# Kernel tuning notes

Hardware: AMD Instinct MI355X
Metric: run time of the kernel (lower is better)

The kernel has to match this reference:

```python
import jax, jax.numpy as jnp
import numpy as np

B, S, D, H, FF = 2, 2048, 1024, 16, 4096
DH = D // H
EPS = 1e-5


def _linear_params(key, din, dout):
    kw, kb = jax.random.split(key)
    lim = 1.0 / np.sqrt(din)
    W = jax.random.uniform(kw, (din, dout), jnp.float32, -lim, lim)
    b = jax.random.uniform(kb, (dout,), jnp.float32, -lim, lim)
    return W, b


def setup_inputs() -> dict:
    key = jax.random.key(0)
    ks = jax.random.split(key, 8)
    x = jax.random.normal(ks[0], (B, S, D), jnp.float32)
    mask = jnp.ones((B, 1, 1, S), jnp.int32)
    wq, bq = _linear_params(ks[1], D, D)
    wk, bk = _linear_params(ks[2], D, D)
    wv, bv = _linear_params(ks[3], D, D)
    w1, b1 = _linear_params(ks[4], D, D)       # linear1 (attn output proj)
    fw1, fb1 = _linear_params(ks[5], D, FF)    # ffn.w_1
    fw2, fb2 = _linear_params(ks[6], FF, D)    # ffn.w_2
    g1 = jnp.ones((D,), jnp.float32); be1 = jnp.zeros((D,), jnp.float32)
    g2 = jnp.ones((D,), jnp.float32); be2 = jnp.zeros((D,), jnp.float32)
    return dict(x=x, mask=mask, wq=wq, bq=bq, wk=wk, bk=bk, wv=wv, bv=bv,
                w1=w1, b1=b1, g1=g1, be1=be1,
                fw1=fw1, fb1=fb1, fw2=fw2, fb2=fb2, g2=g2, be2=be2)


def _layernorm(x, g, b):
    mu = jnp.mean(x, axis=-1, keepdims=True)
    var = jnp.mean(jnp.square(x - mu), axis=-1, keepdims=True)
    return (x - mu) * jax.lax.rsqrt(var + EPS) * g + b


def _encoder(x, mask, wq, bq, wk, bk, wv, bv, w1, b1, g1, be1,
             fw1, fb1, fw2, fb2, g2, be2):
    res = x
    # QKV projections, reshape to [B, H, S, DH]
    q = (x @ wq + bq).reshape(B, S, H, DH).transpose(0, 2, 1, 3)
    k = (x @ wk + bk).reshape(B, S, H, DH).transpose(0, 2, 1, 3)
    v = (x @ wv + bv).reshape(B, S, H, DH).transpose(0, 2, 1, 3)
    scores = jnp.einsum('bhqd,bhkd->bhqk', q, k) / np.sqrt(DH).astype(np.float32)
    scores = jnp.where(mask == 0, jnp.float32(-1e9), scores)
    probs = jax.nn.softmax(scores, axis=-1)  # dropout = identity in eval
    attn = jnp.einsum('bhqk,bhkd->bhqd', probs, v)
    attn = attn.transpose(0, 2, 1, 3).reshape(B, S, D)
    x = _layernorm(attn @ w1 + b1 + res, g1, be1)
    res = x
    ff = jax.nn.relu(x @ fw1 + fb1) @ fw2 + fb2
    return _layernorm(ff + res, g2, be2)


def reference(x, mask, wq, bq, wk, bk, wv, bv, w1, b1, g1, be1,
              fw1, fb1, fw2, fb2, g2, be2):
    return _encoder(x, mask, wq, bq, wk, bk, wv, bv, w1, b1, g1, be1,
                    fw1, fb1, fw2, fb2, g2, be2)
```

## Files before the change

### kernel.cpp

```cpp
#include <hip/hip_runtime.h>
#include <hip/hip_bf16.h>
#include <cstdint>

typedef unsigned short u16;
typedef __attribute__((ext_vector_type(8))) short bf16x8;
typedef __attribute__((ext_vector_type(4))) float f32x4;

#define DEVFN static __device__ __forceinline__

static constexpr int S   = 2048;
static constexpr int D   = 1024;
static constexpr int DHd = 64;
static constexpr int FFd = 4096;
static constexpr int M   = 4096;
static constexpr int LDQ = 3072;

static constexpr float SC2 = 0.18033688f;

DEVFN u16 f2b(float v) {
    union { __hip_bfloat16 h; u16 u; } x;
    x.h = __float2bfloat16(v);
    return x.u;
}

typedef const uint32_t __attribute__((address_space(1)))* gptr_t;
typedef uint32_t __attribute__((address_space(3)))* lptr_t;
DEVFN void load16(const void* g, void* l) {
    __builtin_amdgcn_global_load_lds((gptr_t)g, (lptr_t)l, 16, 0, 0);
}

template<int MODE>
__global__ __launch_bounds__(512, 2)
void gemm256(const u16* __restrict__ A, const u16* __restrict__ BT,
             const float* __restrict__ bias, u16* __restrict__ outp, int N)
{
    constexpr int K = 1024;
    __shared__ __align__(16) u16 Lds[65536];
    const int tid  = threadIdx.x;
    const int lane = tid & 63;
    const int w    = tid >> 6;
    const int wm = w >> 2, wn = w & 3;
    const int g = lane >> 4, c = lane & 15;
    const int c7 = c & 7;
    const int bn0 = blockIdx.x * 256;
    const int bm0 = blockIdx.y * 256;

    const int sr = tid >> 3;
    const int gl = (tid & 7) ^ (sr & 7);
    const u16* Asrc = A  + (size_t)(bm0 + sr) * K + gl * 8;
    const u16* Bsrc = BT + (size_t)(bn0 + sr) * K + gl * 8;
    char* dA = (char*)Lds + (size_t)tid * 16;
    char* dB = dA + 32768;

#define STG_A(BUF, H, KT)                                                       \
    { _Pragma("unroll") for (int Lh = 0; Lh < 2; ++Lh)                          \
        load16(Asrc + (size_t)((H)*128 + Lh*64) * K + (KT)*64,                  \
               dA + (BUF)*65536 + (H)*16384 + Lh*8192); }
#define STG_B(BUF, H, KT)                                                       \
    { _Pragma("unroll") for (int Lh = 0; Lh < 2; ++Lh)                          \
        load16(Bsrc + (size_t)((H)*128 + Lh*64) * K + (KT)*64,                  \
               dB + (BUF)*65536 + (H)*16384 + Lh*8192); }
#define VMCNT(N_) asm volatile("s_waitcnt vmcnt(" #N_ ")" ::: "memory")
#define BAR() { __builtin_amdgcn_s_barrier(); __builtin_amdgcn_sched_barrier(0); }

    const char* lbase = (const char*)Lds;
    auto rdA = [&](int buf, int i, int kk) -> bf16x8 {
        const int half = i >> 2;
        const int lr = (2*(i & 3) + wm) * 16 + c;
        return *(const bf16x8*)(lbase + buf*65536 + half*16384 + lr*128
                                + (((kk<<2) + g) ^ c7) * 16);
    };
    auto rdB = [&](int buf, int j, int kk) -> bf16x8 {
        const int half = j >> 1;
        const int lr = (j & 1)*64 + wn*16 + c;
        return *(const bf16x8*)(lbase + buf*65536 + 32768 + half*16384 + lr*128
                                + (((kk<<2) + g) ^ c7) * 16);
    };

    const f32x4 fz = {0.f, 0.f, 0.f, 0.f};
    f32x4 acc[8][4];
#pragma unroll
    for (int i = 0; i < 8; ++i)
#pragma unroll
        for (int j = 0; j < 4; ++j) acc[i][j] = fz;

    bf16x8 af[4][2], bf[4][2];

    auto body = [&](int cur, int nxt, int kt, bool stage) {
        if (stage) STG_A(nxt, 0, kt + 1);
#pragma unroll
        for (int i = 0; i < 4; ++i)
#pragma unroll
            for (int kk = 0; kk < 2; ++kk) af[i][kk] = rdA(cur, i, kk);
#pragma unroll
        for (int j = 0; j < 2; ++j)
#pragma unroll
            for (int kk = 0; kk < 2; ++kk) bf[j][kk] = rdB(cur, j, kk);
        __builtin_amdgcn_s_setprio(1);
#pragma unroll
        for (int i = 0; i < 4; ++i)
#pragma unroll
            for (int j = 0; j < 2; ++j)
#pragma unroll
                for (int kk = 0; kk < 2; ++kk)
                    acc[i][j] = __builtin_amdgcn_mfma_f32_16x16x32_bf16(
                        af[i][kk], bf[j][kk], acc[i][j], 0, 0, 0);
        __builtin_amdgcn_s_setprio(0);
        if (stage) { VMCNT(4); } else { VMCNT(2); }
        BAR();
        if (stage) STG_B(nxt, 0, kt + 1);
#pragma unroll
        for (int j = 2; j < 4; ++j)
#pragma unroll
            for (int kk = 0; kk < 2; ++kk) bf[j][kk] = rdB(cur, j, kk);
        __builtin_amdgcn_s_setprio(1);
#pragma unroll
        for (int i = 0; i < 4; ++i)
#pragma unroll
            for (int j = 2; j < 4; ++j)
#pragma unroll
                for (int kk = 0; kk < 2; ++kk)
                    acc[i][j] = __builtin_amdgcn_mfma_f32_16x16x32_bf16(
                        af[i][kk], bf[j][kk], acc[i][j], 0, 0, 0);
        __builtin_amdgcn_s_setprio(0);
        if (stage) { VMCNT(4); } else { VMCNT(0); }
        BAR();
        if (stage) STG_B(nxt, 1, kt + 1);
#pragma unroll
        for (int i = 4; i < 8; ++i)
#pragma unroll
            for (int kk = 0; kk < 2; ++kk) af[i - 4][kk] = rdA(cur, i, kk);
        __builtin_amdgcn_s_setprio(1);
#pragma unroll
        for (int i = 4; i < 8; ++i)
#pragma unroll
            for (int j = 0; j < 2; ++j)
#pragma unroll
                for (int kk = 0; kk < 2; ++kk)
                    acc[i][j] = __builtin_amdgcn_mfma_f32_16x16x32_bf16(
                        af[i - 4][kk], bf[j][kk], acc[i][j], 0, 0, 0);
        __builtin_amdgcn_s_setprio(0);
        if (stage) STG_A(nxt, 1, kt + 1);
        __builtin_amdgcn_s_setprio(1);
#pragma unroll
        for (int i = 4; i < 8; ++i)
#pragma unroll
            for (int j = 2; j < 4; ++j)
#pragma unroll
                for (int kk = 0; kk < 2; ++kk)
                    acc[i][j] = __builtin_amdgcn_mfma_f32_16x16x32_bf16(
                        af[i - 4][kk], bf[j][kk], acc[i][j], 0, 0, 0);
        __builtin_amdgcn_s_setprio(0);
        if (stage) { VMCNT(4); BAR(); }
    };

    STG_A(0, 0, 0); STG_B(0, 0, 0); STG_B(0, 1, 0); STG_A(0, 1, 0);
    VMCNT(4);
    BAR();

#pragma unroll 1
    for (int kt = 0; kt < 14; kt += 2) {
        body(0, 1, kt, true);
        body(1, 0, kt + 1, true);
    }
    body(0, 1, 14, true);
    body(1, 0, 15, false);
#undef STG_A
#undef STG_B
#undef VMCNT
#undef BAR

#pragma unroll
    for (int i = 0; i < 8; ++i) {
        const int fm = (i >> 2) * 8 + (i & 3) * 2 + wm;
        const int row = bm0 + fm * 16 + 4 * g;
#pragma unroll
        for (int j = 0; j < 4; ++j) {
            const int fn = (j >> 1) * 8 + (j & 1) * 4 + wn;
            const int col = bn0 + fn * 16 + c;
            const float bv = bias[col];
            const float sc = (MODE == 3 && col < D) ? SC2 : 1.f;
#pragma unroll
            for (int r = 0; r < 4; ++r) {
                float v = acc[i][j][r] + bv;
                if (MODE == 2) v = v > 0.f ? v : 0.f;
                v *= sc;
                outp[(size_t)(row + r) * N + col] = f2b(v);
            }
        }
    }
}

template<int KTOT>
__global__ __launch_bounds__(256, 3)
void gemm_splitk(const u16* __restrict__ A, const u16* __restrict__ BT,
                 float* __restrict__ part)
{
    __shared__ __align__(16) u16 As[128 * 64];
    __shared__ __align__(16) u16 Bs[128 * 64];
    const int tid  = threadIdx.x;
    const int lane = tid & 63;
    const int w    = tid >> 6;
    const int wm = w >> 1, wn = w & 1;
    const int g = lane >> 4, c = lane & 15;
    const int bn0 = blockIdx.x * 128;
    const int bm0 = blockIdx.y * 128;
    const int z   = blockIdx.z;
    const int srow = tid >> 3;
    const int scol = (tid & 7) * 8;

    const f32x4 fz = {0.f, 0.f, 0.f, 0.f};
    f32x4 acc[4][4];
#pragma unroll
    for (int i = 0; i < 4; ++i)
#pragma unroll
        for (int j = 0; j < 4; ++j) acc[i][j] = fz;

    const u16* Ab = A  + (size_t)(bm0 + srow) * KTOT + z * (KTOT/2) + scol;
    const u16* Bb = BT + (size_t)(bn0 + srow) * KTOT + z * (KTOT/2) + scol;
    char* AsB = (char*)As + (size_t)tid * 16;
    char* BsB = (char*)Bs + (size_t)tid * 16;

    for (int kt = 0; kt < KTOT/128; ++kt) {
        const int k0 = kt << 6;
        __syncthreads();
#pragma unroll
        for (int cc = 0; cc < 4; ++cc) {
            load16(Ab + (size_t)(cc * 32) * KTOT + k0, AsB + cc * 4096);
            load16(Bb + (size_t)(cc * 32) * KTOT + k0, BsB + cc * 4096);
        }
        __syncthreads();
#pragma unroll
        for (int kk = 0; kk < 2; ++kk) {
            bf16x8 af[4], bfv[4];
#pragma unroll
            for (int i = 0; i < 4; ++i)
                af[i] = *(const bf16x8*)&As[(wm*64 + i*16 + c) * 64 + kk*32 + g*8];
#pragma unroll
            for (int j = 0; j < 4; ++j)
                bfv[j] = *(const bf16x8*)&Bs[(wn*64 + j*16 + c) * 64 + kk*32 + g*8];
#pragma unroll
            for (int i = 0; i < 4; ++i)
#pragma unroll
                for (int j = 0; j < 4; ++j)
                    acc[i][j] = __builtin_amdgcn_mfma_f32_16x16x32_bf16(
                        af[i], bfv[j], acc[i][j], 0, 0, 0);
        }
    }

    float* outz = part + (size_t)z * M * D;
#pragma unroll
    for (int i = 0; i < 4; ++i) {
        const int row = bm0 + wm*64 + i*16 + g*4;
#pragma unroll
        for (int j = 0; j < 4; ++j) {
            const int col = bn0 + wn*64 + j*16 + c;
#pragma unroll
            for (int r = 0; r < 4; ++r)
                outz[(size_t)(row + r) * D + col] = acc[i][j][r];
        }
    }
}

__global__ __launch_bounds__(256)
void ln_part_fused(const float* __restrict__ part, const float* __restrict__ bias,
                   const float* __restrict__ resid, const float* __restrict__ gam,
                   const float* __restrict__ bet, u16* __restrict__ out_b,
                   float* __restrict__ out_f)
{
    const int row = blockIdx.x;
    const int tid = threadIdx.x;
    __shared__ float red1[4], red2[4];
    const float4 p0 = ((const float4*)(part + (size_t)row * D))[tid];
    const float4 p1 = ((const float4*)(part + (size_t)(M + row) * D))[tid];
    const float4 bv = ((const float4*)bias)[tid];
    const float4 rv = ((const float4*)(resid + (size_t)row * D))[tid];
    const float y0 = p0.x + p1.x + bv.x + rv.x;
    const float y1 = p0.y + p1.y + bv.y + rv.y;
    const float y2 = p0.z + p1.z + bv.z + rv.z;
    const float y3 = p0.w + p1.w + bv.w + rv.w;
    float s1 = y0 + y1 + y2 + y3;
#pragma unroll
    for (int off = 1; off < 64; off <<= 1) s1 += __shfl_xor(s1, off);
    if ((tid & 63) == 0) red1[tid >> 6] = s1;
    __syncthreads();
    const float mu = (red1[0] + red1[1] + red1[2] + red1[3]) * (1.f / 1024.f);
    const float d0 = y0 - mu, d1 = y1 - mu, d2 = y2 - mu, d3 = y3 - mu;
    float s2 = d0*d0 + d1*d1 + d2*d2 + d3*d3;
#pragma unroll
    for (int off = 1; off < 64; off <<= 1) s2 += __shfl_xor(s2, off);
    if ((tid & 63) == 0) red2[tid >> 6] = s2;
    __syncthreads();
    const float var = (red2[0] + red2[1] + red2[2] + red2[3]) * (1.f / 1024.f);
    const float rs = rsqrtf(var + 1e-5f);
    const int c0 = tid * 4;
    const float o0 = d0 * rs * gam[c0+0] + bet[c0+0];
    const float o1 = d1 * rs * gam[c0+1] + bet[c0+1];
    const float o2 = d2 * rs * gam[c0+2] + bet[c0+2];
    const float o3 = d3 * rs * gam[c0+3] + bet[c0+3];
    if (out_b) {
        union { u16 u[4]; uint2 v; } pk;
        pk.u[0] = f2b(o0); pk.u[1] = f2b(o1); pk.u[2] = f2b(o2); pk.u[3] = f2b(o3);
        ((uint2*)(out_b + (size_t)row * D))[tid] = pk.v;
    }
    if (out_f) {
        float4 yv; yv.x = o0; yv.y = o1; yv.z = o2; yv.w = o3;
        ((float4*)(out_f + (size_t)row * D))[tid] = yv;
    }
}

__global__ __launch_bounds__(256, 3)
void attn_fwd9(const u16* __restrict__ QKV, const u16* __restrict__ VT,
               u16* __restrict__ Ob)
{
    __shared__ __align__(16) u16 Ks[3][64 * 64];
    __shared__ __align__(16) u16 Vs[3][64 * 64];
    __shared__ __align__(16) u16 Ps[4][32 * 72];
    const int tid  = threadIdx.x;
    const int lane = tid & 63;
    const int w    = tid >> 6;
    const int g = lane >> 4, c = lane & 15;
    const int bh = blockIdx.y;
    const int b = bh >> 4, h = bh & 15;
    const int q0 = blockIdx.x * 128 + w * 32;

    const u16* Qb = QKV;
    const u16* Kb = QKV + 1024;

    bf16x8 aq[2][2];
#pragma unroll
    for (int rt = 0; rt < 2; ++rt)
#pragma unroll
        for (int kk = 0; kk < 2; ++kk)
            aq[rt][kk] = *(const bf16x8*)&Qb[(size_t)(b*S + q0 + rt*16 + c) * LDQ
                                             + h*DHd + kk*32 + g*8];

    const f32x4 fz = {0.f, 0.f, 0.f, 0.f};
    const short one_b = (short)0x3F80;
    const bf16x8 onesv = {one_b, one_b, one_b, one_b, one_b, one_b, one_b, one_b};
    f32x4 o[2][4];
    f32x4 ol[2];
#pragma unroll
    for (int rt = 0; rt < 2; ++rt) {
        ol[rt] = fz;
#pragma unroll
        for (int j = 0; j < 4; ++j) o[rt][j] = fz;
    }

    const int sr = tid >> 3;
    const int glog = (tid & 7) ^ (sr & 7);
    const u16* Ksrc = Kb + (size_t)(b*S + sr) * LDQ + h*DHd + glog*8;
    const u16* Vsrc = VT + (size_t)(bh*DHd + sr) * S + glog*8;
    char* Kd0 = (char*)&Ks[0][0] + (size_t)tid * 16;
    char* Vd0 = (char*)&Vs[0][0] + (size_t)tid * 16;

#define STAGE(BUFI, kt_)                                                        \
    {                                                                           \
        const int kr0_ = (kt_) * 64;                                            \
        _Pragma("unroll")                                                       \
        for (int cc = 0; cc < 2; ++cc) {                                        \
            load16(Ksrc + (size_t)(kr0_ + cc*32) * LDQ, Kd0 + (BUFI)*8192 + cc*4096); \
            load16(Vsrc + (size_t)(cc*32) * S + kr0_,   Vd0 + (BUFI)*8192 + cc*4096); \
        }                                                                       \
    }
#define WAITBAR(N)                                                              \
    {                                                                           \
        asm volatile("s_waitcnt vmcnt(" #N ")" ::: "memory");                   \
        __builtin_amdgcn_s_barrier();                                           \
        __builtin_amdgcn_sched_barrier(0);                                      \
    }

    u16* pw = &Ps[w][0];
    const int c7 = c & 7;

    auto tile_body = [&](const u16* K0, const u16* V0) {
        bf16x8 bk[4][2];
#pragma unroll
        for (int j = 0; j < 4; ++j)
#pragma unroll
            for (int kk = 0; kk < 2; ++kk)
                bk[j][kk] = *(const bf16x8*)&K0[(j*16 + c) * 64 + (((kk<<2)+g) ^ c7) * 8];

#pragma unroll
        for (int rt = 0; rt < 2; ++rt) {
            f32x4 sv[4];
            __builtin_amdgcn_s_setprio(1);
#pragma unroll
            for (int j = 0; j < 4; ++j) {
                sv[j] = fz;
#pragma unroll
                for (int kk = 0; kk < 2; ++kk)
                    sv[j] = __builtin_amdgcn_mfma_f32_16x16x32_bf16(
                        bk[j][kk], aq[rt][kk], sv[j], 0, 0, 0);
            }
            __builtin_amdgcn_s_setprio(0);

#pragma unroll
            for (int j = 0; j < 4; ++j) {
                const float p0 = exp2f(sv[j][0]);
                const float p1 = exp2f(sv[j][1]);
                const float p2 = exp2f(sv[j][2]);
                const float p3 = exp2f(sv[j][3]);
                union { u16 u[4]; uint2 v; } pk;
                pk.u[0] = f2b(p0); pk.u[1] = f2b(p1);
                pk.u[2] = f2b(p2); pk.u[3] = f2b(p3);
                *(uint2*)&pw[(rt*16 + c) * 72 + j*16 + g*4] = pk.v;
            }
        }

        __builtin_amdgcn_s_setprio(1);
#pragma unroll
        for (int st = 0; st < 2; ++st) {
            bf16x8 bv[4];
#pragma unroll
            for (int j = 0; j < 4; ++j)
                bv[j] = *(const bf16x8*)&V0[(j*16 + c) * 64 + (((st<<2)+g) ^ c7) * 8];
#pragma unroll
            for (int rt = 0; rt < 2; ++rt) {
                const bf16x8 ap = *(const bf16x8*)&pw[(rt*16 + c) * 72 + st*32 + g*8];
#pragma unroll
                for (int j = 0; j < 4; ++j)
                    o[rt][j] = __builtin_amdgcn_mfma_f32_16x16x32_bf16(
                        ap, bv[j], o[rt][j], 0, 0, 0);
                ol[rt] = __builtin_amdgcn_mfma_f32_16x16x32_bf16(
                    ap, onesv, ol[rt], 0, 0, 0);
            }
        }
        __builtin_amdgcn_s_setprio(0);
    };

    STAGE(0, 0);
    STAGE(1, 1);
    WAITBAR(4);

    int kt = 0;
#pragma unroll 1
    for (int it = 0; it < 10; ++it, kt += 3) {
        STAGE(2, kt + 2); tile_body(&Ks[0][0], &Vs[0][0]); WAITBAR(4);
        STAGE(0, kt + 3); tile_body(&Ks[1][0], &Vs[1][0]); WAITBAR(4);
        STAGE(1, kt + 4); tile_body(&Ks[2][0], &Vs[2][0]); WAITBAR(4);
    }
    tile_body(&Ks[0][0], &Vs[0][0]); WAITBAR(0);
    tile_body(&Ks[1][0], &Vs[1][0]);
#undef STAGE
#undef WAITBAR

#pragma unroll
    for (int rt = 0; rt < 2; ++rt) {
#pragma unroll
        for (int r = 0; r < 4; ++r) {
            const float rl = __builtin_amdgcn_rcpf(ol[rt][r]);
            const size_t row = (size_t)(b*S + q0 + rt*16 + 4*g + r) * D + h*DHd;
#pragma unroll
            for (int j = 0; j < 4; ++j)
                Ob[row + j*16 + c] = f2b(o[rt][j][r] * rl);
        }
    }
}

__global__ void cast_bf16_k(const float* __restrict__ in, u16* __restrict__ out) {
    const int i = blockIdx.x * blockDim.x + threadIdx.x;
    const float4 v = ((const float4*)in)[i];
    union { u16 u[4]; uint2 p; } pk;
    pk.u[0] = f2b(v.x); pk.u[1] = f2b(v.y); pk.u[2] = f2b(v.z); pk.u[3] = f2b(v.w);
    ((uint2*)out)[i] = pk.p;
}

__global__ void concat3_k(const float* __restrict__ a, const float* __restrict__ b,
                          const float* __restrict__ c, float* __restrict__ o) {
    const int i = blockIdx.x * blockDim.x + threadIdx.x;
    o[i] = i < 1024 ? a[i] : (i < 2048 ? b[i - 1024] : c[i - 2048]);
}

__global__ void transpose_cast_k(const float* __restrict__ src, u16* __restrict__ dst,
                                 int R, int C) {
    __shared__ float tile[32][33];
    const int c0 = blockIdx.x * 32, r0 = blockIdx.y * 32;
    const int tx = threadIdx.x, ty = threadIdx.y;
#pragma unroll
    for (int i = 0; i < 4; ++i)
        tile[ty + i*8][tx] = src[(size_t)(r0 + ty + i*8) * C + c0 + tx];
    __syncthreads();
#pragma unroll
    for (int i = 0; i < 4; ++i)
        dst[(size_t)(c0 + ty + i*8) * R + r0 + tx] = f2b(tile[tx][ty + i*8]);
}

__global__ __launch_bounds__(256)
void v_transpose_k(const u16* __restrict__ Vp, u16* __restrict__ VT) {
    __shared__ u16 tile[64][65];
    const int bh = blockIdx.y, b = bh >> 4, h = bh & 15;
    const int s0 = blockIdx.x * 64;
    const int tid = threadIdx.x;
#pragma unroll
    for (int i = 0; i < 16; ++i) {
        const int e = tid + i * 256, r = e >> 6, cc = e & 63;
        tile[r][cc] = Vp[(size_t)(b*S + s0 + r) * LDQ + h*DHd + cc];
    }
    __syncthreads();
#pragma unroll
    for (int i = 0; i < 16; ++i) {
        const int e = tid + i * 256, d = e >> 6, sc = e & 63;
        VT[(size_t)(bh*DHd + d) * S + s0 + sc] = tile[sc][d];
    }
}

extern "C" void kernel_launch(void* const* d_in, const int* in_sizes, int n_in,
                              void* d_out, int out_size, void* d_ws, size_t ws_size,
                              hipStream_t stream)
{
    (void)in_sizes; (void)n_in; (void)out_size; (void)ws_size;
    const float* x   = (const float*)d_in[0];
    const float* wq  = (const float*)d_in[2];
    const float* bq  = (const float*)d_in[3];
    const float* wk  = (const float*)d_in[4];
    const float* bk  = (const float*)d_in[5];
    const float* wv  = (const float*)d_in[6];
    const float* bv  = (const float*)d_in[7];
    const float* w1  = (const float*)d_in[8];
    const float* b1  = (const float*)d_in[9];
    const float* g1  = (const float*)d_in[10];
    const float* be1 = (const float*)d_in[11];
    const float* fw1 = (const float*)d_in[12];
    const float* fb1 = (const float*)d_in[13];
    const float* fw2 = (const float*)d_in[14];
    const float* fb2 = (const float*)d_in[15];
    const float* g2  = (const float*)d_in[16];
    const float* be2 = (const float*)d_in[17];

    char* ws = (char*)d_ws;
    size_t off = 0;
    auto alloc = [&](size_t bytes) -> void* {
        void* p = ws + off;
        off += (bytes + 255) & ~(size_t)255;
        return p;
    };
    u16*   Xb    = (u16*)alloc((size_t)M * D * 2);
    u16*   WqkvT = (u16*)alloc((size_t)3 * D * D * 2);
    u16*   W1T   = (u16*)alloc((size_t)D * D * 2);
    u16*   F1T   = (u16*)alloc((size_t)D * FFd * 2);
    u16*   F2T   = (u16*)alloc((size_t)D * FFd * 2);
    u16*   QKV   = (u16*)alloc((size_t)M * LDQ * 2);
    u16*   VTh   = (u16*)alloc((size_t)M * D * 2);
    u16*   Ob    = (u16*)alloc((size_t)M * D * 2);
    float* x1f   = (float*)alloc((size_t)M * D * 4);
    u16*   x1b   = (u16*)alloc((size_t)M * D * 2);
    u16*   Hb    = (u16*)alloc((size_t)M * FFd * 2);
    float* bqkv  = (float*)alloc((size_t)LDQ * 4);

    float* Part = (float*)QKV;

    cast_bf16_k<<<dim3(M * D / 1024), dim3(256), 0, stream>>>(x, Xb);
    dim3 tb(32, 8);
    transpose_cast_k<<<dim3(D/32, D/32),   tb, 0, stream>>>(wq,  WqkvT,                 D, D);
    transpose_cast_k<<<dim3(D/32, D/32),   tb, 0, stream>>>(wk,  WqkvT + (size_t)D*D,   D, D);
    transpose_cast_k<<<dim3(D/32, D/32),   tb, 0, stream>>>(wv,  WqkvT + (size_t)2*D*D, D, D);
    transpose_cast_k<<<dim3(D/32, D/32),   tb, 0, stream>>>(w1,  W1T, D, D);
    transpose_cast_k<<<dim3(FFd/32, D/32), tb, 0, stream>>>(fw1, F1T, D, FFd);
    transpose_cast_k<<<dim3(D/32, FFd/32), tb, 0, stream>>>(fw2, F2T, FFd, D);
    concat3_k<<<dim3(LDQ/256), dim3(256), 0, stream>>>(bq, bk, bv, bqkv);

    gemm256<3><<<dim3(LDQ/256, M/256), 512, 0, stream>>>(Xb, WqkvT, bqkv, QKV, LDQ);

    v_transpose_k<<<dim3(S/64, 32), 256, 0, stream>>>(QKV + 2048, VTh);

    attn_fwd9<<<dim3(S/128, 32), 256, 0, stream>>>(QKV, VTh, Ob);

    gemm_splitk<D><<<dim3(D/128, M/128, 2), 256, 0, stream>>>(Ob, W1T, Part);

    ln_part_fused<<<dim3(M), 256, 0, stream>>>(Part, b1, x, g1, be1, x1b, x1f);

    gemm256<2><<<dim3(FFd/256, M/256), 512, 0, stream>>>(x1b, F1T, fb1, Hb, FFd);

    gemm_splitk<FFd><<<dim3(D/128, M/128, 2), 256, 0, stream>>>(Hb, F2T, Part);

    ln_part_fused<<<dim3(M), 256, 0, stream>>>(Part, fb2, x1f, g2, be2, nullptr, (float*)d_out);
}
```

Before: 257.2 us.

## Run FFN down-projection on 256-tile GEMM with four-way split-K

The gemm256 kernel gains a K-stride template parameter and a split-K mode that writes fp32 partials per blockIdx.z. The FFN second GEMM now uses this kernel with K=4096 split into four 1024-long chunks, replacing the 128-tile split-2 kernel. The LayerNorm reducer is templated on the number of partials. Workspace buffers are reordered so that the fp32 partial buffer, which aliases QKV, can hold four partials across buffers that are dead by then. The aim is the higher arithmetic efficiency of the large-tile kernel, at the cost of doubling partial-sum memory traffic.

```diff
diff --git a/kernel.cpp b/kernel.cpp
--- a/kernel.cpp
+++ b/kernel.cpp
@@ -29,12 +29,11 @@
     __builtin_amdgcn_global_load_lds((gptr_t)g, (lptr_t)l, 16, 0, 0);
 }
 
-template<int MODE>
+template<int MODE, int KS>
 __global__ __launch_bounds__(512, 2)
 void gemm256(const u16* __restrict__ A, const u16* __restrict__ BT,
-             const float* __restrict__ bias, u16* __restrict__ outp, int N)
+             const float* __restrict__ bias, void* __restrict__ outp, int N)
 {
-    constexpr int K = 1024;
     __shared__ __align__(16) u16 Lds[65536];
     const int tid  = threadIdx.x;
     const int lane = tid & 63;
@@ -44,21 +43,23 @@
     const int c7 = c & 7;
     const int bn0 = blockIdx.x * 256;
     const int bm0 = blockIdx.y * 256;
+    const int z   = (MODE == 4) ? (int)blockIdx.z : 0;
+    const size_t kofs = (size_t)z * 1024;
 
     const int sr = tid >> 3;
     const int gl = (tid & 7) ^ (sr & 7);
-    const u16* Asrc = A  + (size_t)(bm0 + sr) * K + gl * 8;
-    const u16* Bsrc = BT + (size_t)(bn0 + sr) * K + gl * 8;
+    const u16* Asrc = A  + (size_t)(bm0 + sr) * KS + kofs + gl * 8;
+    const u16* Bsrc = BT + (size_t)(bn0 + sr) * KS + kofs + gl * 8;
     char* dA = (char*)Lds + (size_t)tid * 16;
     char* dB = dA + 32768;
 
 #define STG_A(BUF, H, KT)                                                       \
     { _Pragma("unroll") for (int Lh = 0; Lh < 2; ++Lh)                          \
-        load16(Asrc + (size_t)((H)*128 + Lh*64) * K + (KT)*64,                  \
+        load16(Asrc + (size_t)((H)*128 + Lh*64) * KS + (KT)*64,                 \
                dA + (BUF)*65536 + (H)*16384 + Lh*8192); }
 #define STG_B(BUF, H, KT)                                                       \
     { _Pragma("unroll") for (int Lh = 0; Lh < 2; ++Lh)                          \
-        load16(Bsrc + (size_t)((H)*128 + Lh*64) * K + (KT)*64,                  \
+        load16(Bsrc + (size_t)((H)*128 + Lh*64) * KS + (KT)*64,                 \
                dB + (BUF)*65536 + (H)*16384 + Lh*8192); }
 #define VMCNT(N_) asm volatile("s_waitcnt vmcnt(" #N_ ")" ::: "memory")
 #define BAR() { __builtin_amdgcn_s_barrier(); __builtin_amdgcn_sched_barrier(0); }
@@ -170,22 +171,39 @@
 #undef VMCNT
 #undef BAR
 
-#pragma unroll
-    for (int i = 0; i < 8; ++i) {
-        const int fm = (i >> 2) * 8 + (i & 3) * 2 + wm;
-        const int row = bm0 + fm * 16 + 4 * g;
-#pragma unroll
-        for (int j = 0; j < 4; ++j) {
-            const int fn = (j >> 1) * 8 + (j & 1) * 4 + wn;
-            const int col = bn0 + fn * 16 + c;
-            const float bv = bias[col];
-            const float sc = (MODE == 3 && col < D) ? SC2 : 1.f;
-#pragma unroll
-            for (int r = 0; r < 4; ++r) {
-                float v = acc[i][j][r] + bv;
-                if (MODE == 2) v = v > 0.f ? v : 0.f;
-                v *= sc;
-                outp[(size_t)(row + r) * N + col] = f2b(v);
+    if (MODE == 4) {
+        float* outz = (float*)outp + (size_t)z * M * D;
+#pragma unroll
+        for (int i = 0; i < 8; ++i) {
+            const int fm = (i >> 2) * 8 + (i & 3) * 2 + wm;
+            const int row = bm0 + fm * 16 + 4 * g;
+#pragma unroll
+            for (int j = 0; j < 4; ++j) {
+                const int fn = (j >> 1) * 8 + (j & 1) * 4 + wn;
+                const int col = bn0 + fn * 16 + c;
+#pragma unroll
+                for (int r = 0; r < 4; ++r)
+                    outz[(size_t)(row + r) * D + col] = acc[i][j][r];
+            }
+        }
+    } else {
+#pragma unroll
+        for (int i = 0; i < 8; ++i) {
+            const int fm = (i >> 2) * 8 + (i & 3) * 2 + wm;
+            const int row = bm0 + fm * 16 + 4 * g;
+#pragma unroll
+            for (int j = 0; j < 4; ++j) {
+                const int fn = (j >> 1) * 8 + (j & 1) * 4 + wn;
+                const int col = bn0 + fn * 16 + c;
+                const float bv = bias[col];
+                const float sc = (MODE == 3 && col < D) ? SC2 : 1.f;
+#pragma unroll
+                for (int r = 0; r < 4; ++r) {
+                    float v = acc[i][j][r] + bv;
+                    if (MODE == 2) v = v > 0.f ? v : 0.f;
+                    v *= sc;
+                    ((u16*)outp)[(size_t)(row + r) * N + col] = f2b(v);
+                }
             }
         }
     }
@@ -262,6 +280,7 @@
     }
 }
 
+template<int NPART>
 __global__ __launch_bounds__(256)
 void ln_part_fused(const float* __restrict__ part, const float* __restrict__ bias,
                    const float* __restrict__ resid, const float* __restrict__ gam,
@@ -271,14 +290,14 @@
     const int row = blockIdx.x;
     const int tid = threadIdx.x;
     __shared__ float red1[4], red2[4];
-    const float4 p0 = ((const float4*)(part + (size_t)row * D))[tid];
-    const float4 p1 = ((const float4*)(part + (size_t)(M + row) * D))[tid];
     const float4 bv = ((const float4*)bias)[tid];
     const float4 rv = ((const float4*)(resid + (size_t)row * D))[tid];
-    const float y0 = p0.x + p1.x + bv.x + rv.x;
-    const float y1 = p0.y + p1.y + bv.y + rv.y;
-    const float y2 = p0.z + p1.z + bv.z + rv.z;
-    const float y3 = p0.w + p1.w + bv.w + rv.w;
+    float y0 = bv.x + rv.x, y1 = bv.y + rv.y, y2 = bv.z + rv.z, y3 = bv.w + rv.w;
+#pragma unroll
+    for (int p = 0; p < NPART; ++p) {
+        const float4 pv = ((const float4*)(part + (size_t)(p * M + row) * D))[tid];
+        y0 += pv.x; y1 += pv.y; y2 += pv.z; y3 += pv.w;
+    }
     float s1 = y0 + y1 + y2 + y3;
 #pragma unroll
     for (int off = 1; off < 64; off <<= 1) s1 += __shfl_xor(s1, off);
@@ -535,14 +554,14 @@
         off += (bytes + 255) & ~(size_t)255;
         return p;
     };
+    u16*   QKV   = (u16*)alloc((size_t)M * LDQ * 2);
+    u16*   VTh   = (u16*)alloc((size_t)M * D * 2);
+    u16*   Ob    = (u16*)alloc((size_t)M * D * 2);
     u16*   Xb    = (u16*)alloc((size_t)M * D * 2);
     u16*   WqkvT = (u16*)alloc((size_t)3 * D * D * 2);
     u16*   W1T   = (u16*)alloc((size_t)D * D * 2);
     u16*   F1T   = (u16*)alloc((size_t)D * FFd * 2);
     u16*   F2T   = (u16*)alloc((size_t)D * FFd * 2);
-    u16*   QKV   = (u16*)alloc((size_t)M * LDQ * 2);
-    u16*   VTh   = (u16*)alloc((size_t)M * D * 2);
-    u16*   Ob    = (u16*)alloc((size_t)M * D * 2);
     float* x1f   = (float*)alloc((size_t)M * D * 4);
     u16*   x1b   = (u16*)alloc((size_t)M * D * 2);
     u16*   Hb    = (u16*)alloc((size_t)M * FFd * 2);
@@ -560,7 +579,7 @@
     transpose_cast_k<<<dim3(D/32, FFd/32), tb, 0, stream>>>(fw2, F2T, FFd, D);
     concat3_k<<<dim3(LDQ/256), dim3(256), 0, stream>>>(bq, bk, bv, bqkv);
 
-    gemm256<3><<<dim3(LDQ/256, M/256), 512, 0, stream>>>(Xb, WqkvT, bqkv, QKV, LDQ);
+    gemm256<3, D><<<dim3(LDQ/256, M/256), 512, 0, stream>>>(Xb, WqkvT, bqkv, QKV, LDQ);
 
     v_transpose_k<<<dim3(S/64, 32), 256, 0, stream>>>(QKV + 2048, VTh);
 
@@ -568,11 +587,11 @@
 
     gemm_splitk<D><<<dim3(D/128, M/128, 2), 256, 0, stream>>>(Ob, W1T, Part);
 
-    ln_part_fused<<<dim3(M), 256, 0, stream>>>(Part, b1, x, g1, be1, x1b, x1f);
-
-    gemm256<2><<<dim3(FFd/256, M/256), 512, 0, stream>>>(x1b, F1T, fb1, Hb, FFd);
-
-    gemm_splitk<FFd><<<dim3(D/128, M/128, 2), 256, 0, stream>>>(Hb, F2T, Part);
-
-    ln_part_fused<<<dim3(M), 256, 0, stream>>>(Part, fb2, x1f, g2, be2, nullptr, (float*)d_out);
-}
+    ln_part_fused<2><<<dim3(M), 256, 0, stream>>>(Part, b1, x, g1, be1, x1b, x1f);
+
+    gemm256<2, D><<<dim3(FFd/256, M/256), 512, 0, stream>>>(x1b, F1T, fb1, Hb, FFd);
+
+    gemm256<4, FFd><<<dim3(D/256, M/256, 4), 512, 0, stream>>>(Hb, F2T, nullptr, Part, D);
+
+    ln_part_fused<4><<<dim3(M), 256, 0, stream>>>(Part, fb2, x1f, g2, be2, nullptr, (float*)d_out);
+}
```

Result: faster. 247.5 us (-3.8%).
